# Kernel optimization log

Hardware: AMD Instinct MI355X
Metric: run time of the kernel (lower is better)

## Reference

```python
import jax, jax.numpy as jnp
import numpy as np

B = 8192       # Monte Carlo paths
NSTEP = 30     # Euler time steps
D = 100        # z_dim / number of assets
H1 = 110
H2 = 110
T = NSTEP - 1  # number of subnets
DT = np.float32(1.0 / NSTEP)
R = np.float32(0.05)   # riskfree
EPS = np.float32(1e-3) # Keras BatchNormalization epsilon


def setup_inputs() -> dict:
    key = jax.random.key(0)
    ks = jax.random.split(key, 25)
    f = jnp.float32
    X = jax.random.normal(ks[0], (B, NSTEP, D), f)
    DWs = jax.random.normal(ks[1], (B, NSTEP, D), f) * jnp.sqrt(DT)
    sigmas = jax.random.uniform(ks[2], (D,), f, 0.1, 0.4)
    y_init = jax.random.uniform(ks[3], (1,), f, 0.0, 1.0)
    z_init = jax.random.uniform(ks[4], (1, D), f, -0.1, 0.1)
    W1 = jax.random.normal(ks[5], (T, D, H1), f) / np.sqrt(D).astype(np.float32)
    W2 = jax.random.normal(ks[6], (T, H1, H2), f) / np.sqrt(H1).astype(np.float32)
    W3 = jax.random.normal(ks[7], (T, H2, D), f) / np.sqrt(H2).astype(np.float32)
    dims = [D, H1, H2, D]
    bn = {}
    for j, dim in enumerate(dims):
        bn[f"g{j}"] = 1.0 + 0.1 * jax.random.normal(ks[8 + 4 * j], (T, dim), f)
        bn[f"b{j}"] = 0.05 * jax.random.normal(ks[9 + 4 * j], (T, dim), f)
        bn[f"m{j}"] = 0.1 * jax.random.normal(ks[10 + 4 * j], (T, dim), f)
        bn[f"v{j}"] = jax.random.uniform(ks[11 + 4 * j], (T, dim), f, 0.5, 1.5)
    return dict(X=X, DWs=DWs, sigmas=sigmas, y_init=y_init, z_init=z_init,
                W1=W1, W2=W2, W3=W3, **bn)


def _bn(x, g, b, m, v):
    # Keras BatchNormalization, inference mode
    return (x - m) * jax.lax.rsqrt(v + EPS) * g + b


def _subnet(x, p):
    (w1, w2, w3, g0, b0, m0, v0, g1, b1, m1, v1,
     g2, b2, m2, v2, g3, b3, m3, v3) = p
    x = _bn(x, g0, b0, m0, v0)
    x = jax.nn.relu(x @ w1)
    x = _bn(x, g1, b1, m1, v1)
    x = jax.nn.relu(x @ w2)
    x = _bn(x, g2, b2, m2, v2)
    x = x @ w3
    return _bn(x, g3, b3, m3, v3)


def reference(X, DWs, sigmas, y_init, z_init, W1, W2, W3,
              g0, b0, m0, v0, g1, b1, m1, v1,
              g2, b2, m2, v2, g3, b3, m3, v3):
    nb = X.shape[0]
    Y0 = jnp.ones((nb, 1), X.dtype) * y_init            # [B,1]
    Z0 = jnp.ones((nb, 1), X.dtype) * z_init            # [B,D]

    def step(carry, xs):
        Y, Z = carry
        Xi, Xn, DWi, p = xs
        Y = Y + R * Y * DT + jnp.sum(sigmas * Xi * Z * DWi, axis=1, keepdims=True)
        Z = _subnet(Xn, p)
        return (Y, Z), None

    params = (W1, W2, W3, g0, b0, m0, v0, g1, b1, m1, v1,
              g2, b2, m2, v2, g3, b3, m3, v3)  # each leading dim T
    xs = (jnp.moveaxis(X[:, :T], 1, 0),        # [T,B,D]
          jnp.moveaxis(X[:, 1:T + 1], 1, 0),   # [T,B,D]
          jnp.moveaxis(DWs[:, :T], 1, 0),      # [T,B,D]
          params)
    (Y, Z), _ = jax.lax.scan(step, (Y0, Z0), xs)
    # final step: X[:,-2,:] with DWs[:,-1,:]
    Y = Y + R * Y * DT + jnp.sum(sigmas * X[:, -2, :] * Z * DWs[:, -1, :],
                                 axis=1, keepdims=True)
    return Y
```

## Files before the change

### kernel.cpp

```cpp
#include <hip/hip_runtime.h>

typedef unsigned short ushort_t;
typedef __attribute__((ext_vector_type(8))) short s16x8;
typedef __attribute__((ext_vector_type(4))) float f32x4;

#define B_PATHS 8192
#define NSTEP   30
#define DD      100
#define HH      110
#define TT      29
#define ROWSTR  3000
#define LDK     136
#define WFRAGSZ 14336
#define DT_C    (1.0f/30.0f)
#define R_C     0.05f
#define EPS_C   1e-3f

__device__ __forceinline__ ushort_t f2bf(float f) {
  unsigned u = __float_as_uint(f);
  u = u + 0x7FFFu + ((u >> 16) & 1u);
  return (ushort_t)(u >> 16);
}
__device__ __forceinline__ float bf2f(ushort_t u) {
  return __uint_as_float(((unsigned)u) << 16);
}

__global__ void prep_kernel(const float* __restrict__ W1, const float* __restrict__ W2,
                            const float* __restrict__ W3,
                            const float* g0, const float* b0, const float* m0, const float* v0,
                            const float* g1, const float* b1, const float* m1, const float* v1,
                            const float* g2, const float* b2, const float* m2, const float* v2,
                            const float* g3, const float* b3, const float* m3, const float* v3,
                            ushort_t* __restrict__ wprep, float* __restrict__ bprep)
{
  const int mat = blockIdx.x, t = blockIdx.y, tid = threadIdx.x;
  __shared__ __align__(16) float wsh[110*110];
  __shared__ float sin_[112], hin_[112], sout_[112], hout_[112];

  int Kr, Nr; const float* W; const float *g, *bb, *mm, *vv;
  if (mat == 0)      { Kr = 100; Nr = 110; W = W1 + t*11000; g = g0+t*100; bb = b0+t*100; mm = m0+t*100; vv = v0+t*100; }
  else if (mat == 1) { Kr = 110; Nr = 110; W = W2 + t*12100; g = g1+t*110; bb = b1+t*110; mm = m1+t*110; vv = v1+t*110; }
  else               { Kr = 110; Nr = 100; W = W3 + t*11000; g = g2+t*110; bb = b2+t*110; mm = m2+t*110; vv = v2+t*110; }

  if (tid < Kr) {
    float s = g[tid] * rsqrtf(vv[tid] + EPS_C);
    sin_[tid] = s; hin_[tid] = bb[tid] - mm[tid]*s;
  }
  if (mat == 2 && tid < Nr) {
    float s = g3[t*100+tid] * rsqrtf(v3[t*100+tid] + EPS_C);
    sout_[tid] = s; hout_[tid] = b3[t*100+tid] - m3[t*100+tid]*s;
  }
  {
    const int n4 = (Kr*Nr) >> 2;
    for (int i = tid; i < n4; i += 256)
      ((float4*)wsh)[i] = ((const float4*)W)[i];
  }
  __syncthreads();

  if (tid < 128) {
    float c = 0.f;
    if (tid < Nr) {
      for (int k = 0; k < Kr; ++k) c += hin_[k] * wsh[k*Nr + tid];
      if (mat == 2) c = c * sout_[tid] + hout_[tid];
    }
    bprep[(t*3 + mat)*128 + tid] = c;
  }

  ushort_t* wo = wprep + (size_t)(t*3 + mat) * WFRAGSZ;
  for (int ch = tid; ch < 1792; ch += 256) {
    const int lane = ch & 63, ntkb = ch >> 6;
    const int nt = ntkb % 7, kb = ntkb / 7;
    const int n  = nt*16 + (lane & 15);
    const int k0 = kb*32 + (lane >> 4)*8;
    ushort_t tmp[8];
#pragma unroll
    for (int j = 0; j < 8; ++j) {
      const int k = k0 + j;
      float v = 0.f;
      if (n < Nr && k < Kr) {
        v = sin_[k] * wsh[k*Nr + n];
        if (mat == 2) v *= sout_[n];
      }
      tmp[j] = f2bf(v);
    }
    ushort4 lo; lo.x = tmp[0]; lo.y = tmp[1]; lo.z = tmp[2]; lo.w = tmp[3];
    ushort4 hi; hi.x = tmp[4]; hi.y = tmp[5]; hi.z = tmp[6]; hi.w = tmp[7];
    *(ushort4*)(wo + ch*8)     = lo;
    *(ushort4*)(wo + ch*8 + 4) = hi;
  }
}

__device__ __forceinline__ void mlp_stage16(ushort_t* act, const ushort_t* wbuf,
                                            const float* __restrict__ biasg,
                                            int wrow, int lane, int lrow, int quad, bool relu)
{
  f32x4 acc[7];
  const f32x4 z4 = {0.f, 0.f, 0.f, 0.f};
#pragma unroll
  for (int nt = 0; nt < 7; ++nt) acc[nt] = z4;

  s16x8 a[4];
#pragma unroll
  for (int kb = 0; kb < 4; ++kb)
    a[kb] = *(const s16x8*)(act + (wrow + lrow)*LDK + kb*32 + quad*8);

#pragma unroll
  for (int kb = 0; kb < 4; ++kb) {
    s16x8 b[7];
#pragma unroll
    for (int nt = 0; nt < 7; ++nt)
      b[nt] = *(const s16x8*)(wbuf + ((kb*7 + nt)*64 + lane)*8);
#pragma unroll
    for (int nt = 0; nt < 7; ++nt)
      acc[nt] = __builtin_amdgcn_mfma_f32_16x16x32_bf16(a[kb], b[nt], acc[nt], 0, 0, 0);
  }

#pragma unroll
  for (int nt = 0; nt < 7; ++nt) {
    const int col = nt*16 + lrow;
    const float bv = biasg[col];
#pragma unroll
    for (int r = 0; r < 4; ++r) {
      float u = acc[nt][r] + bv;
      if (relu) u = u > 0.f ? u : 0.f;
      act[(wrow + quad*4 + r)*LDK + col] = f2bf(u);
    }
  }
#pragma unroll
  for (int r = 0; r < 4; ++r)
    act[(wrow + quad*4 + r)*LDK + 112 + lrow] = 0;
}

__global__ __launch_bounds__(256, 3)
void subnet_kernel(const float* __restrict__ X, const float* __restrict__ DW,
                   const float* __restrict__ sigmas,
                   const ushort_t* __restrict__ wprep, const float* __restrict__ bprep,
                   float* __restrict__ sbuf)
{
  __shared__ __align__(16) ushort_t act[64*LDK];
  __shared__ __align__(16) ushort_t wbuf[WFRAGSZ];

  const int tid  = threadIdx.x;
  const int t    = blockIdx.y;
  const int m0   = blockIdx.x * 64;
  const int lane = tid & 63;
  const int wrow = (tid >> 6) * 16;
  const int lrow = lane & 15, quad = lane >> 4;

  const ushort_t* wf = wprep + (size_t)(t*3) * WFRAGSZ;
  const float*    bg = bprep + (t*3) * 128;

  s16x8 wst[7];
#pragma unroll
  for (int j = 0; j < 7; ++j)
    wst[j] = *(const s16x8*)(wf + (j*256 + tid)*8);

  for (int jj = tid; jj < 64*32; jj += 256) {
    const int r = jj >> 5, c = jj & 31;
    ushort4 u; u.x = 0; u.y = 0; u.z = 0; u.w = 0;
    if (c < 25) {
      const float4 v = *(const float4*)(X + (size_t)(m0 + r)*ROWSTR + (t+1)*DD + c*4);
      u.x = f2bf(v.x); u.y = f2bf(v.y); u.z = f2bf(v.z); u.w = f2bf(v.w);
    }
    *(ushort4*)(act + r*LDK + c*4) = u;
  }

#pragma unroll
  for (int j = 0; j < 7; ++j)
    *(s16x8*)(wbuf + (j*256 + tid)*8) = wst[j];
  __syncthreads();

#pragma unroll
  for (int j = 0; j < 7; ++j)
    wst[j] = *(const s16x8*)(wf + WFRAGSZ + (j*256 + tid)*8);
  mlp_stage16(act, wbuf, bg, wrow, lane, lrow, quad, true);
  __syncthreads();
#pragma unroll
  for (int j = 0; j < 7; ++j)
    *(s16x8*)(wbuf + (j*256 + tid)*8) = wst[j];
  __syncthreads();

#pragma unroll
  for (int j = 0; j < 7; ++j)
    wst[j] = *(const s16x8*)(wf + 2*WFRAGSZ + (j*256 + tid)*8);
  mlp_stage16(act, wbuf, bg + 128, wrow, lane, lrow, quad, true);
  __syncthreads();
#pragma unroll
  for (int j = 0; j < 7; ++j)
    *(s16x8*)(wbuf + (j*256 + tid)*8) = wst[j];
  __syncthreads();

  mlp_stage16(act, wbuf, bg + 256, wrow, lane, lrow, quad, false);

  {
    const int row  = wrow + (lane >> 2);
    const int part = lane & 3;
    const int b    = m0 + row;
    const int xt   = (t == TT - 1) ? (NSTEP - 2) : (t + 1);
    const float* xr = X  + (size_t)b*ROWSTR + xt*DD;
    const float* dr = DW + (size_t)b*ROWSTR + (t+1)*DD;
    float p = 0.f;
#pragma unroll
    for (int g = part; g < 25; g += 4) {
      const float4 xv = *(const float4*)(xr + g*4);
      const float4 dv = *(const float4*)(dr + g*4);
      const float4 sg = *(const float4*)(sigmas + g*4);
      const ushort4 zu = *(const ushort4*)(act + row*LDK + g*4);
      p += sg.x*xv.x*dv.x*bf2f(zu.x);
      p += sg.y*xv.y*dv.y*bf2f(zu.y);
      p += sg.z*xv.z*dv.z*bf2f(zu.z);
      p += sg.w*xv.w*dv.w*bf2f(zu.w);
    }
    p += __shfl_xor(p, 1, 64);
    p += __shfl_xor(p, 2, 64);
    if (part == 0)
      sbuf[(size_t)(t+1)*B_PATHS + b] = p;
  }
}

__global__ __launch_bounds__(256)
void y_kernel(const float* __restrict__ X, const float* __restrict__ DW,
              const float* __restrict__ sigmas, const float* __restrict__ y_init,
              const float* __restrict__ z_init, const float* __restrict__ sbuf,
              float* __restrict__ out)
{
  const int tid  = threadIdx.x;
  const int row  = tid >> 3, part = tid & 7;
  const int b    = blockIdx.x * 32 + row;
  const float* xr = X + (size_t)b * ROWSTR;
  const float* dr = DW + (size_t)b * ROWSTR;
  float p = 0.f;
#pragma unroll
  for (int g = part; g < 25; g += 8) {
    const float4 xv = *(const float4*)(xr + g*4);
    const float4 dv = *(const float4*)(dr + g*4);
    const float4 sg = *(const float4*)(sigmas + g*4);
    const float4 zv = *(const float4*)(z_init + g*4);
    p += sg.x*xv.x*zv.x*dv.x;
    p += sg.y*xv.y*zv.y*dv.y;
    p += sg.z*xv.z*zv.z*dv.z;
    p += sg.w*xv.w*zv.w*dv.w;
  }
  p += __shfl_xor(p, 1, 64);
  p += __shfl_xor(p, 2, 64);
  p += __shfl_xor(p, 4, 64);

  const float G = 1.f + R_C*DT_C;
  float ss = 0.f;
#pragma unroll
  for (int tau = 1 + part; tau < NSTEP; tau += 8)
    ss += sbuf[(size_t)tau*B_PATHS + b] * __powf(G, (float)(NSTEP - 1 - tau));
  ss += __shfl_xor(ss, 1, 64);
  ss += __shfl_xor(ss, 2, 64);
  ss += __shfl_xor(ss, 4, 64);

  if (part == 0)
    out[b] = y_init[0]*__powf(G, 30.f) + p*__powf(G, 29.f) + ss;
}

extern "C" void kernel_launch(void* const* d_in, const int* in_sizes, int n_in,
                              void* d_out, int out_size, void* d_ws, size_t ws_size,
                              hipStream_t stream) {
  const float* X      = (const float*)d_in[0];
  const float* DWs    = (const float*)d_in[1];
  const float* sigmas = (const float*)d_in[2];
  const float* y_init = (const float*)d_in[3];
  const float* z_init = (const float*)d_in[4];
  const float* W1     = (const float*)d_in[5];
  const float* W2     = (const float*)d_in[6];
  const float* W3     = (const float*)d_in[7];
  const float* bn[16];
  for (int i = 0; i < 16; ++i) bn[i] = (const float*)d_in[8 + i];

  char* ws = (char*)d_ws;
  ushort_t* wprep = (ushort_t*)ws;
  float*    bprep = (float*)(ws + 2494464);
  float*    sbuf  = (float*)(ws + 2539008);
  float*    out   = (float*)d_out;

  prep_kernel<<<dim3(3, TT), 256, 0, stream>>>(
      W1, W2, W3,
      bn[0], bn[1], bn[2], bn[3],  bn[4], bn[5], bn[6], bn[7],
      bn[8], bn[9], bn[10], bn[11], bn[12], bn[13], bn[14], bn[15],
      wprep, bprep);
  subnet_kernel<<<dim3(B_PATHS/64, TT), 256, 0, stream>>>(
      X, DWs, sigmas, wprep, bprep, sbuf);
  y_kernel<<<dim3(B_PATHS/32), 256, 0, stream>>>(
      X, DWs, sigmas, y_init, z_init, sbuf, out);
}
```

Measured before the change: 322.2 us.

## Make subnet kernel loop over chunks of timesteps with prefetched inputs

Each block now processes a contiguous range of 7-8 timesteps instead of one, cutting the grid from 29 to 4 in y. Within the loop, the next step's X tile, weight fragments and the current DW slice are loaded into registers while the MLP stages run, hiding global latency. Launch bounds drop to 2 waves per SIMD to fit the extra prefetch registers. The cost is fewer blocks for parallelism (512 total) and lower occupancy.

```diff
diff --git a/kernel.cpp b/kernel.cpp
--- a/kernel.cpp
+++ b/kernel.cpp
@@ -131,7 +131,7 @@
     act[(wrow + quad*4 + r)*LDK + 112 + lrow] = 0;
 }
 
-__global__ __launch_bounds__(256, 3)
+__global__ __launch_bounds__(256, 2)
 void subnet_kernel(const float* __restrict__ X, const float* __restrict__ DW,
                    const float* __restrict__ sigmas,
                    const ushort_t* __restrict__ wprep, const float* __restrict__ bprep,
@@ -141,80 +141,132 @@
   __shared__ __align__(16) ushort_t wbuf[WFRAGSZ];
 
   const int tid  = threadIdx.x;
-  const int t    = blockIdx.y;
   const int m0   = blockIdx.x * 64;
+  const int cy   = blockIdx.y;
+  const int t0   = cy ? (1 + cy*7) : 0;
+  const int t1   = t0 + (cy == 0 ? 8 : 7);
   const int lane = tid & 63;
   const int wrow = (tid >> 6) * 16;
   const int lrow = lane & 15, quad = lane >> 4;
-
-  const ushort_t* wf = wprep + (size_t)(t*3) * WFRAGSZ;
-  const float*    bg = bprep + (t*3) * 128;
+  const int erow = wrow + (lane >> 2), epart = lane & 3;
 
   s16x8 wst[7];
-#pragma unroll
-  for (int j = 0; j < 7; ++j)
-    wst[j] = *(const s16x8*)(wf + (j*256 + tid)*8);
-
-  for (int jj = tid; jj < 64*32; jj += 256) {
-    const int r = jj >> 5, c = jj & 31;
-    ushort4 u; u.x = 0; u.y = 0; u.z = 0; u.w = 0;
-    if (c < 25) {
-      const float4 v = *(const float4*)(X + (size_t)(m0 + r)*ROWSTR + (t+1)*DD + c*4);
-      u.x = f2bf(v.x); u.y = f2bf(v.y); u.z = f2bf(v.z); u.w = f2bf(v.w);
-    }
-    *(ushort4*)(act + r*LDK + c*4) = u;
-  }
-
-#pragma unroll
-  for (int j = 0; j < 7; ++j)
-    *(s16x8*)(wbuf + (j*256 + tid)*8) = wst[j];
-  __syncthreads();
-
-#pragma unroll
-  for (int j = 0; j < 7; ++j)
-    wst[j] = *(const s16x8*)(wf + WFRAGSZ + (j*256 + tid)*8);
-  mlp_stage16(act, wbuf, bg, wrow, lane, lrow, quad, true);
-  __syncthreads();
-#pragma unroll
-  for (int j = 0; j < 7; ++j)
-    *(s16x8*)(wbuf + (j*256 + tid)*8) = wst[j];
-  __syncthreads();
-
-#pragma unroll
-  for (int j = 0; j < 7; ++j)
-    wst[j] = *(const s16x8*)(wf + 2*WFRAGSZ + (j*256 + tid)*8);
-  mlp_stage16(act, wbuf, bg + 128, wrow, lane, lrow, quad, true);
-  __syncthreads();
-#pragma unroll
-  for (int j = 0; j < 7; ++j)
-    *(s16x8*)(wbuf + (j*256 + tid)*8) = wst[j];
-  __syncthreads();
-
-  mlp_stage16(act, wbuf, bg + 256, wrow, lane, lrow, quad, false);
 
   {
-    const int row  = wrow + (lane >> 2);
-    const int part = lane & 3;
-    const int b    = m0 + row;
-    const int xt   = (t == TT - 1) ? (NSTEP - 2) : (t + 1);
-    const float* xr = X  + (size_t)b*ROWSTR + xt*DD;
-    const float* dr = DW + (size_t)b*ROWSTR + (t+1)*DD;
-    float p = 0.f;
-#pragma unroll
-    for (int g = part; g < 25; g += 4) {
-      const float4 xv = *(const float4*)(xr + g*4);
-      const float4 dv = *(const float4*)(dr + g*4);
-      const float4 sg = *(const float4*)(sigmas + g*4);
-      const ushort4 zu = *(const ushort4*)(act + row*LDK + g*4);
-      p += sg.x*xv.x*dv.x*bf2f(zu.x);
-      p += sg.y*xv.y*dv.y*bf2f(zu.y);
-      p += sg.z*xv.z*dv.z*bf2f(zu.z);
-      p += sg.w*xv.w*dv.w*bf2f(zu.w);
-    }
-    p += __shfl_xor(p, 1, 64);
-    p += __shfl_xor(p, 2, 64);
-    if (part == 0)
-      sbuf[(size_t)(t+1)*B_PATHS + b] = p;
+    const ushort_t* wf0 = wprep + (size_t)(t0*3) * WFRAGSZ;
+#pragma unroll
+    for (int j = 0; j < 7; ++j)
+      wst[j] = *(const s16x8*)(wf0 + (j*256 + tid)*8);
+    for (int jj = tid; jj < 64*32; jj += 256) {
+      const int r = jj >> 5, c = jj & 31;
+      ushort4 u; u.x = 0; u.y = 0; u.z = 0; u.w = 0;
+      if (c < 25) {
+        const float4 v = *(const float4*)(X + (size_t)(m0 + r)*ROWSTR + (t0+1)*DD + c*4);
+        u.x = f2bf(v.x); u.y = f2bf(v.y); u.z = f2bf(v.z); u.w = f2bf(v.w);
+      }
+      *(ushort4*)(act + r*LDK + c*4) = u;
+    }
+#pragma unroll
+    for (int j = 0; j < 7; ++j)
+      *(s16x8*)(wbuf + (j*256 + tid)*8) = wst[j];
+    __syncthreads();
+  }
+
+  for (int t = t0; t < t1; ++t) {
+    const ushort_t* wf = wprep + (size_t)(t*3) * WFRAGSZ;
+    const float*    bg = bprep + (t*3) * 128;
+    const bool has_next = (t + 1 < t1);
+
+#pragma unroll
+    for (int j = 0; j < 7; ++j)
+      wst[j] = *(const s16x8*)(wf + WFRAGSZ + (j*256 + tid)*8);
+
+    float4 dreg[7];
+    {
+      const float* dr = DW + (size_t)(m0 + erow)*ROWSTR + (t+1)*DD;
+#pragma unroll
+      for (int i = 0; i < 7; ++i) {
+        const int g = epart + i*4;
+        if (g < 25) dreg[i] = *(const float4*)(dr + g*4);
+        else { dreg[i].x = 0.f; dreg[i].y = 0.f; dreg[i].z = 0.f; dreg[i].w = 0.f; }
+      }
+    }
+    float4 xreg[8];
+    if (has_next) {
+#pragma unroll
+      for (int i = 0; i < 8; ++i) {
+        const int jj = tid + i*256, r = jj >> 5, c = jj & 31;
+        if (c < 25)
+          xreg[i] = *(const float4*)(X + (size_t)(m0 + r)*ROWSTR + (t+2)*DD + c*4);
+        else { xreg[i].x = 0.f; xreg[i].y = 0.f; xreg[i].z = 0.f; xreg[i].w = 0.f; }
+      }
+    }
+
+    mlp_stage16(act, wbuf, bg, wrow, lane, lrow, quad, true);
+    __syncthreads();
+#pragma unroll
+    for (int j = 0; j < 7; ++j)
+      *(s16x8*)(wbuf + (j*256 + tid)*8) = wst[j];
+    __syncthreads();
+
+#pragma unroll
+    for (int j = 0; j < 7; ++j)
+      wst[j] = *(const s16x8*)(wf + 2*WFRAGSZ + (j*256 + tid)*8);
+    mlp_stage16(act, wbuf, bg + 128, wrow, lane, lrow, quad, true);
+    __syncthreads();
+#pragma unroll
+    for (int j = 0; j < 7; ++j)
+      *(s16x8*)(wbuf + (j*256 + tid)*8) = wst[j];
+    __syncthreads();
+
+    if (has_next) {
+      const ushort_t* wfn = wprep + (size_t)((t+1)*3) * WFRAGSZ;
+#pragma unroll
+      for (int j = 0; j < 7; ++j)
+        wst[j] = *(const s16x8*)(wfn + (j*256 + tid)*8);
+    }
+    mlp_stage16(act, wbuf, bg + 256, wrow, lane, lrow, quad, false);
+
+    {
+      const int xt = (t == TT - 1) ? (NSTEP - 2) : (t + 1);
+      const float* xr = X + (size_t)(m0 + erow)*ROWSTR + xt*DD;
+      float p = 0.f;
+#pragma unroll
+      for (int i = 0; i < 7; ++i) {
+        const int g = epart + i*4;
+        if (g < 25) {
+          const float4 xv = *(const float4*)(xr + g*4);
+          const float4 sg = *(const float4*)(sigmas + g*4);
+          const ushort4 zu = *(const ushort4*)(act + erow*LDK + g*4);
+          p += sg.x*xv.x*dreg[i].x*bf2f(zu.x);
+          p += sg.y*xv.y*dreg[i].y*bf2f(zu.y);
+          p += sg.z*xv.z*dreg[i].z*bf2f(zu.z);
+          p += sg.w*xv.w*dreg[i].w*bf2f(zu.w);
+        }
+      }
+      p += __shfl_xor(p, 1, 64);
+      p += __shfl_xor(p, 2, 64);
+      if (epart == 0)
+        sbuf[(size_t)(t+1)*B_PATHS + (m0 + erow)] = p;
+    }
+
+    if (has_next) {
+      __syncthreads();
+#pragma unroll
+      for (int i = 0; i < 8; ++i) {
+        const int jj = tid + i*256, r = jj >> 5, c = jj & 31;
+        ushort4 u; u.x = 0; u.y = 0; u.z = 0; u.w = 0;
+        if (c < 25) {
+          u.x = f2bf(xreg[i].x); u.y = f2bf(xreg[i].y);
+          u.z = f2bf(xreg[i].z); u.w = f2bf(xreg[i].w);
+        }
+        *(ushort4*)(act + r*LDK + c*4) = u;
+      }
+#pragma unroll
+      for (int j = 0; j < 7; ++j)
+        *(s16x8*)(wbuf + (j*256 + tid)*8) = wst[j];
+      __syncthreads();
+    }
   }
 }
 
@@ -283,7 +335,7 @@
       bn[0], bn[1], bn[2], bn[3],  bn[4], bn[5], bn[6], bn[7],
       bn[8], bn[9], bn[10], bn[11], bn[12], bn[13], bn[14], bn[15],
       wprep, bprep);
-  subnet_kernel<<<dim3(B_PATHS/64, TT), 256, 0, stream>>>(
+  subnet_kernel<<<dim3(B_PATHS/64, 4), 256, 0, stream>>>(
       X, DWs, sigmas, wprep, bprep, sbuf);
   y_kernel<<<dim3(B_PATHS/32), 256, 0, stream>>>(
       X, DWs, sigmas, y_init, z_init, sbuf, out);
```

Result: slower. 337.2 us (+4.7%).

## Pre-transpose X to bf16 time-major layout and precompute sigma*X*DW products

Applied to the files above, without the earlier changes.

Adds a transpose kernel that reads each path's X and DW rows once, writes X as bf16 in a time-major padded [t][b][128] layout, and precomputes sigma*X*DW products as bf16. The subnet kernel then loads contiguous bf16 activation tiles and the epilogue reads the precomputed products instead of three fp32 streams. This aims to cut strided fp32 global traffic in the main kernel, at the cost of an extra pass over X and DW plus roughly 110MB of workspace writes and reads. The products are also rounded to bf16, which loses precision.

```diff
diff --git a/kernel.cpp b/kernel.cpp
--- a/kernel.cpp
+++ b/kernel.cpp
@@ -16,6 +16,12 @@
 #define R_C     0.05f
 #define EPS_C   1e-3f
 
+#define WS_WPREP 0u
+#define WS_BPREP 2494464u
+#define WS_SBUF  2539008u
+#define WS_XBT   3522048u
+#define WS_PBUF  64339456u
+
 __device__ __forceinline__ ushort_t f2bf(float f) {
   unsigned u = __float_as_uint(f);
   u = u + 0x7FFFu + ((u >> 16) & 1u);
@@ -90,6 +96,56 @@
   }
 }
 
+__global__ __launch_bounds__(256, 4)
+void transpose_kernel(const float* __restrict__ X, const float* __restrict__ DW,
+                      const float* __restrict__ sigmas,
+                      ushort_t* __restrict__ xbt, ushort_t* __restrict__ pbuf)
+{
+  __shared__ __align__(16) float xs[3000];
+  __shared__ __align__(16) float ds[3000];
+  __shared__ float sig[128];
+  const int tid = threadIdx.x;
+  if (tid < 128) sig[tid] = (tid < 100) ? sigmas[tid] : 0.f;
+
+  const int b0 = blockIdx.x * 8;
+  for (int p = 0; p < 8; ++p) {
+    const int b = b0 + p;
+    __syncthreads();
+    const float4* xr = (const float4*)(X  + (size_t)b * ROWSTR);
+    const float4* dr = (const float4*)(DW + (size_t)b * ROWSTR);
+    for (int i = tid; i < 750; i += 256) {
+      ((float4*)xs)[i] = xr[i];
+      ((float4*)ds)[i] = dr[i];
+    }
+    __syncthreads();
+
+    for (int i = tid; i < 464; i += 256) {
+      const int t0 = i >> 4, c = i & 15;
+      s16x8 u;
+#pragma unroll
+      for (int j = 0; j < 8; ++j) {
+        const int col = c*8 + j;
+        const float v = (col < 100) ? xs[(t0+1)*100 + col] : 0.f;
+        u[j] = (short)f2bf(v);
+      }
+      *(s16x8*)(xbt + ((size_t)t0*B_PATHS + b)*128 + c*8) = u;
+    }
+    for (int i = tid; i < 750; i += 256) {
+      const int tau = i / 25, g = i % 25;
+      const int xt  = tau ? (tau < 29 ? tau : 28) : 0;
+      const float* xp = xs + xt*100 + g*4;
+      const float* dp = ds + tau*100 + g*4;
+      const float* sp = sig + g*4;
+      ushort4 u;
+      u.x = f2bf(sp[0]*xp[0]*dp[0]);
+      u.y = f2bf(sp[1]*xp[1]*dp[1]);
+      u.z = f2bf(sp[2]*xp[2]*dp[2]);
+      u.w = f2bf(sp[3]*xp[3]*dp[3]);
+      *(ushort4*)(pbuf + ((size_t)tau*B_PATHS + b)*100 + g*4) = u;
+    }
+  }
+}
+
 __device__ __forceinline__ void mlp_stage16(ushort_t* act, const ushort_t* wbuf,
                                             const float* __restrict__ biasg,
                                             int wrow, int lane, int lrow, int quad, bool relu)
@@ -132,8 +188,7 @@
 }
 
 __global__ __launch_bounds__(256, 3)
-void subnet_kernel(const float* __restrict__ X, const float* __restrict__ DW,
-                   const float* __restrict__ sigmas,
+void subnet_kernel(const ushort_t* __restrict__ xbt, const ushort_t* __restrict__ pbuf,
                    const ushort_t* __restrict__ wprep, const float* __restrict__ bprep,
                    float* __restrict__ sbuf)
 {
@@ -155,14 +210,13 @@
   for (int j = 0; j < 7; ++j)
     wst[j] = *(const s16x8*)(wf + (j*256 + tid)*8);
 
-  for (int jj = tid; jj < 64*32; jj += 256) {
-    const int r = jj >> 5, c = jj & 31;
-    ushort4 u; u.x = 0; u.y = 0; u.z = 0; u.w = 0;
-    if (c < 25) {
-      const float4 v = *(const float4*)(X + (size_t)(m0 + r)*ROWSTR + (t+1)*DD + c*4);
-      u.x = f2bf(v.x); u.y = f2bf(v.y); u.z = f2bf(v.z); u.w = f2bf(v.w);
-    }
-    *(ushort4*)(act + r*LDK + c*4) = u;
+  {
+    const ushort_t* xsrc = xbt + ((size_t)t*B_PATHS + m0)*128;
+#pragma unroll
+    for (int i = 0; i < 4; ++i) {
+      const int j = tid + i*256, r = j >> 4, c = j & 15;
+      *(s16x8*)(act + r*LDK + c*8) = *(const s16x8*)(xsrc + r*128 + c*8);
+    }
   }
 
 #pragma unroll
@@ -193,53 +247,42 @@
   mlp_stage16(act, wbuf, bg + 256, wrow, lane, lrow, quad, false);
 
   {
-    const int row  = wrow + (lane >> 2);
-    const int part = lane & 3;
-    const int b    = m0 + row;
-    const int xt   = (t == TT - 1) ? (NSTEP - 2) : (t + 1);
-    const float* xr = X  + (size_t)b*ROWSTR + xt*DD;
-    const float* dr = DW + (size_t)b*ROWSTR + (t+1)*DD;
+    const int erow = wrow + (lane >> 2), epart = lane & 3;
+    const int b    = m0 + erow;
+    const ushort_t* pr = pbuf + ((size_t)(t+1)*B_PATHS + b)*100;
     float p = 0.f;
 #pragma unroll
-    for (int g = part; g < 25; g += 4) {
-      const float4 xv = *(const float4*)(xr + g*4);
-      const float4 dv = *(const float4*)(dr + g*4);
-      const float4 sg = *(const float4*)(sigmas + g*4);
-      const ushort4 zu = *(const ushort4*)(act + row*LDK + g*4);
-      p += sg.x*xv.x*dv.x*bf2f(zu.x);
-      p += sg.y*xv.y*dv.y*bf2f(zu.y);
-      p += sg.z*xv.z*dv.z*bf2f(zu.z);
-      p += sg.w*xv.w*dv.w*bf2f(zu.w);
+    for (int i = 0; i < 7; ++i) {
+      const int g = epart + i*4;
+      if (g < 25) {
+        const ushort4 pu = *(const ushort4*)(pr + g*4);
+        const ushort4 zu = *(const ushort4*)(act + erow*LDK + g*4);
+        p += bf2f(pu.x)*bf2f(zu.x) + bf2f(pu.y)*bf2f(zu.y)
+           + bf2f(pu.z)*bf2f(zu.z) + bf2f(pu.w)*bf2f(zu.w);
+      }
     }
     p += __shfl_xor(p, 1, 64);
     p += __shfl_xor(p, 2, 64);
-    if (part == 0)
+    if (epart == 0)
       sbuf[(size_t)(t+1)*B_PATHS + b] = p;
   }
 }
 
 __global__ __launch_bounds__(256)
-void y_kernel(const float* __restrict__ X, const float* __restrict__ DW,
-              const float* __restrict__ sigmas, const float* __restrict__ y_init,
+void y_kernel(const ushort_t* __restrict__ pbuf, const float* __restrict__ y_init,
               const float* __restrict__ z_init, const float* __restrict__ sbuf,
               float* __restrict__ out)
 {
   const int tid  = threadIdx.x;
   const int row  = tid >> 3, part = tid & 7;
   const int b    = blockIdx.x * 32 + row;
-  const float* xr = X + (size_t)b * ROWSTR;
-  const float* dr = DW + (size_t)b * ROWSTR;
+  const ushort_t* pr = pbuf + (size_t)b*100;
   float p = 0.f;
 #pragma unroll
   for (int g = part; g < 25; g += 8) {
-    const float4 xv = *(const float4*)(xr + g*4);
-    const float4 dv = *(const float4*)(dr + g*4);
-    const float4 sg = *(const float4*)(sigmas + g*4);
-    const float4 zv = *(const float4*)(z_init + g*4);
-    p += sg.x*xv.x*zv.x*dv.x;
-    p += sg.y*xv.y*zv.y*dv.y;
-    p += sg.z*xv.z*zv.z*dv.z;
-    p += sg.w*xv.w*zv.w*dv.w;
+    const ushort4 pu = *(const ushort4*)(pr + g*4);
+    const float4  zv = *(const float4*)(z_init + g*4);
+    p += bf2f(pu.x)*zv.x + bf2f(pu.y)*zv.y + bf2f(pu.z)*zv.z + bf2f(pu.w)*zv.w;
   }
   p += __shfl_xor(p, 1, 64);
   p += __shfl_xor(p, 2, 64);
@@ -273,9 +316,11 @@
   for (int i = 0; i < 16; ++i) bn[i] = (const float*)d_in[8 + i];
 
   char* ws = (char*)d_ws;
-  ushort_t* wprep = (ushort_t*)ws;
-  float*    bprep = (float*)(ws + 2494464);
-  float*    sbuf  = (float*)(ws + 2539008);
+  ushort_t* wprep = (ushort_t*)(ws + WS_WPREP);
+  float*    bprep = (float*)   (ws + WS_BPREP);
+  float*    sbuf  = (float*)   (ws + WS_SBUF);
+  ushort_t* xbt   = (ushort_t*)(ws + WS_XBT);
+  ushort_t* pbuf  = (ushort_t*)(ws + WS_PBUF);
   float*    out   = (float*)d_out;
 
   prep_kernel<<<dim3(3, TT), 256, 0, stream>>>(
@@ -283,8 +328,10 @@
       bn[0], bn[1], bn[2], bn[3],  bn[4], bn[5], bn[6], bn[7],
       bn[8], bn[9], bn[10], bn[11], bn[12], bn[13], bn[14], bn[15],
       wprep, bprep);
+  transpose_kernel<<<dim3(B_PATHS/8), 256, 0, stream>>>(
+      X, DWs, sigmas, xbt, pbuf);
   subnet_kernel<<<dim3(B_PATHS/64, TT), 256, 0, stream>>>(
-      X, DWs, sigmas, wprep, bprep, sbuf);
+      xbt, pbuf, wprep, bprep, sbuf);
   y_kernel<<<dim3(B_PATHS/32), 256, 0, stream>>>(
-      X, DWs, sigmas, y_init, z_init, sbuf, out);
-}
+      pbuf, y_init, z_init, sbuf, out);
+}
```

Result: slower. 358.4 us (+11.2%).
